# Optimization experiments

Measured on AMD Instinct MI355X. Metric: run time of the kernel, lower is better.

The kernel has to match this reference:

```python
import jax, jax.numpy as jnp
import numpy as np

H = 16  # n_heads (from init_kwargs)


def l2norm(x, eps=1e-6):
    return x * jax.lax.rsqrt(jnp.sum(x * x, axis=-1, keepdims=True) + eps)


def causal_conv1d(x, w, b):
    # depthwise causal conv: x (B,T,D), w (D,k), b (D,). Matches torch
    # Conv1d(d,d,k,groups=d,padding=k-1) followed by [:, :, :T] truncation.
    T = x.shape[1]
    k = w.shape[1]
    xp = jnp.pad(x, ((0, 0), (k - 1, 0), (0, 0)))
    y = b
    for j in range(k):  # k=4 taps, fixed small loop
        y = y + xp[:, j:j + T, :] * w[:, j]
    return y


def setup_inputs():
    key = jax.random.key(0)
    ks = jax.random.split(key, 16)
    B, T, D, kc = 2, 2048, 1024, 4
    d = D // H
    s = 1.0 / np.sqrt(D)
    return {
        "x": jax.random.normal(ks[0], (B, T, D), jnp.float32),
        "Wq": jax.random.normal(ks[1], (D, D), jnp.float32) * s,
        "Wk": jax.random.normal(ks[2], (D, D), jnp.float32) * s,
        "Wv": jax.random.normal(ks[3], (D, D), jnp.float32) * s,
        "Wo": jax.random.normal(ks[4], (D, D), jnp.float32) * s,
        "Wg": jax.random.normal(ks[5], (D, D), jnp.float32) * s,
        "Wb": jax.random.normal(ks[6], (D, H), jnp.float32) * s,
        "cq_w": jax.random.normal(ks[7], (D, kc), jnp.float32) * 0.3,
        "cq_b": jax.random.normal(ks[8], (D,), jnp.float32) * 0.1,
        "ck_w": jax.random.normal(ks[9], (D, kc), jnp.float32) * 0.3,
        "ck_b": jax.random.normal(ks[10], (D,), jnp.float32) * 0.1,
        "cv_w": jax.random.normal(ks[11], (D, kc), jnp.float32) * 0.3,
        "cv_b": jax.random.normal(ks[12], (D,), jnp.float32) * 0.1,
        "nw": jnp.ones((d,), jnp.float32),
    }


def reference(x, Wq, Wk, Wv, Wo, Wg, Wb, cq_w, cq_b, ck_w, ck_b, cv_w, cv_b, nw):
    B, T, D = x.shape
    d = D // H
    q = l2norm(jax.nn.silu(causal_conv1d(x @ Wq, cq_w, cq_b)).reshape(B, T, H, d))
    q = q / jnp.sqrt(jnp.asarray(d, x.dtype))
    k = l2norm(jax.nn.silu(causal_conv1d(x @ Wk, ck_w, ck_b)).reshape(B, T, H, d))
    v = jax.nn.silu(causal_conv1d(x @ Wv, cv_w, cv_b)).reshape(B, T, H, d)
    gate = (x @ Wg).reshape(B, T, H, d)
    beta = jax.nn.sigmoid(x @ Wb)[..., None]  # (B,T,H,1)

    def step(S, qkvb):
        q_t, k_t, v_t, b_t = qkvb  # (B,H,d), (B,H,d), (B,H,d), (B,H,1)
        err = (v_t - jnp.einsum('bhk,bhkv->bhv', k_t, S)) * b_t
        S = S + jnp.einsum('bhk,bhv->bhkv', k_t, err)
        o_t = jnp.einsum('bhk,bhkv->bhv', q_t, S)
        return S, o_t

    S0 = jnp.zeros((B, H, d, d), x.dtype)
    xs = (q.transpose(1, 0, 2, 3), k.transpose(1, 0, 2, 3),
          v.transpose(1, 0, 2, 3), beta.transpose(1, 0, 2, 3))
    _, oT = jax.lax.scan(step, S0, xs)
    o = oT.transpose(1, 0, 2, 3)  # (B,T,H,d)
    # RMSNorm over head_dim
    o = o * jax.lax.rsqrt(jnp.mean(o * o, axis=-1, keepdims=True) + 1e-5) * nw
    o = o * jax.nn.silu(gate)
    return o.reshape(B, T, D) @ Wo
```

## Files before the change

### kernel.cpp

```cpp
#include <hip/hip_runtime.h>
#include <hip/hip_bf16.h>

typedef __attribute__((ext_vector_type(8))) short short8;
typedef __attribute__((ext_vector_type(4))) float f32x4;

#define TSEQ 2048
#define DMODEL 1024
#define NH 16
#define HD 64
#define PLANE 4194304

__device__ __forceinline__ ushort f2bf(float f) {
    union { float f; unsigned int u; } c; c.f = f;
    unsigned int u = c.u + 0x7fffu + ((c.u >> 16) & 1u);
    return (ushort)(u >> 16);
}

__device__ __forceinline__ float bf2f(ushort u) {
    union { unsigned int i; float f; } c; c.i = ((unsigned int)u) << 16;
    return c.f;
}

__device__ __forceinline__ void split2(float x, ushort& h, ushort& l) {
    h = f2bf(x);
    float r = x - bf2f(h);
    l = f2bf(r);
}

__device__ __forceinline__ float silu_f(float y) {
    return y / (1.f + __expf(-y));
}

__device__ __forceinline__ void gl_lds16(const float* g, float* l) {
    __builtin_amdgcn_global_load_lds(
        (__attribute__((address_space(1))) void*)g,
        (__attribute__((address_space(3))) void*)l, 16, 0, 0);
}
__device__ __forceinline__ void gl_lds16u(const ushort* g, ushort* l) {
    __builtin_amdgcn_global_load_lds(
        (__attribute__((address_space(1))) void*)g,
        (__attribute__((address_space(3))) void*)l, 16, 0, 0);
}

__global__ void gdn_cvt_x(const float* __restrict__ x, ushort* __restrict__ xb) {
    int i = blockIdx.x * 256 + threadIdx.x;
    float4 v = ((const float4*)x)[i];
    ushort4 o;
    o.x = f2bf(v.x); o.y = f2bf(v.y); o.z = f2bf(v.z); o.w = f2bf(v.w);
    ((ushort4*)xb)[i] = o;
}

__global__ void gdn_cvt_w(const float* __restrict__ Wq, const float* __restrict__ Wk,
                          const float* __restrict__ Wv, const float* __restrict__ Wg,
                          const float* __restrict__ Wo, ushort* __restrict__ wt) {
    __shared__ float tile[32][33];
    int z = blockIdx.z;
    const float* W = (z == 0) ? Wq : (z == 1) ? Wk : (z == 2) ? Wv : (z == 3) ? Wg : Wo;
    int n0 = blockIdx.x * 32, k0 = blockIdx.y * 32;
    int tx = threadIdx.x, ty = threadIdx.y;
    #pragma unroll
    for (int j = 0; j < 32; j += 8)
        tile[ty + j][tx] = W[(size_t)(k0 + ty + j) * DMODEL + n0 + tx];
    __syncthreads();
    ushort* o = wt + (size_t)z * DMODEL * DMODEL;
    #pragma unroll
    for (int j = 0; j < 32; j += 8)
        o[(size_t)(n0 + ty + j) * DMODEL + k0 + tx] = f2bf(tile[tx][ty + j]);
}

__global__ void gdn_beta(const float* __restrict__ x, const float* __restrict__ Wb,
                         float* __restrict__ betaT) {
    __shared__ float xs[16][DMODEL];
    int tid = threadIdx.x;
    int m0 = blockIdx.x * 16;
    #pragma unroll
    for (int i = 0; i < 16; i++) {
        int idx = i * 256 + tid;
        int row = idx >> 8, c4 = idx & 255;
        *(float4*)&xs[row][c4 * 4] =
            *(const float4*)&x[(size_t)(m0 + row) * DMODEL + c4 * 4];
    }
    __syncthreads();
    int h = tid & 15, mi = tid >> 4;
    float acc = 0.f;
    for (int k = 0; k < DMODEL; ++k)
        acc += xs[mi][k] * Wb[k * NH + h];
    int m = m0 + mi;
    int b = m >> 11, t = m & (TSEQ - 1);
    betaT[((b * NH + h) << 11) + t] = 1.f / (1.f + __expf(-acc));
}

#define BK 32
__global__ __launch_bounds__(256) void gdn_gemm(const ushort* __restrict__ A,
                                                const ushort* __restrict__ Bt,
                                                float* __restrict__ outF,
                                                size_t planeStride) {
    __shared__ ushort As[128 * BK];
    __shared__ ushort Bs[128 * BK];
    int tid = threadIdx.x;
    int lane = tid & 63, wid = tid >> 6;
    int wm = wid & 1, wn = wid >> 1;
    int l15 = lane & 15, quad = lane >> 4;
    int bm = blockIdx.x, bn = blockIdx.y;
    const int K = DMODEL;

    int e0 = wid, e1 = wid + 4;
    int srow0 = e0 * 16 + (lane >> 2), srow1 = e1 * 16 + (lane >> 2);
    int scol = (lane & 3) * 8;
    const ushort* Ag0 = A + (size_t)(bm * 128 + srow0) * K + scol;
    const ushort* Ag1 = A + (size_t)(bm * 128 + srow1) * K + scol;
    const ushort* Bg0 = Bt + (size_t)(bn * 128 + srow0) * K + scol;
    const ushort* Bg1 = Bt + (size_t)(bn * 128 + srow1) * K + scol;
    ushort* Al0 = As + e0 * 512;
    ushort* Al1 = As + e1 * 512;
    ushort* Bl0 = Bs + e0 * 512;
    ushort* Bl1 = Bs + e1 * 512;

    f32x4 acc[4][4];
    #pragma unroll
    for (int i = 0; i < 4; i++)
        #pragma unroll
        for (int j = 0; j < 4; j++)
            acc[i][j] = (f32x4){0.f, 0.f, 0.f, 0.f};

    for (int kt = 0; kt < K; kt += BK) {
        __syncthreads();
        gl_lds16u(Ag0 + kt, Al0);
        gl_lds16u(Ag1 + kt, Al1);
        gl_lds16u(Bg0 + kt, Bl0);
        gl_lds16u(Bg1 + kt, Bl1);
        __syncthreads();
        short8 af[4], bf[4];
        #pragma unroll
        for (int i = 0; i < 4; i++) {
            af[i] = *(const short8*)&As[(wm * 64 + i * 16 + l15) * BK + quad * 8];
            bf[i] = *(const short8*)&Bs[(wn * 64 + i * 16 + l15) * BK + quad * 8];
        }
        #pragma unroll
        for (int mt = 0; mt < 4; mt++)
            #pragma unroll
            for (int nt = 0; nt < 4; nt++)
                acc[mt][nt] = __builtin_amdgcn_mfma_f32_16x16x32_bf16(
                    af[mt], bf[nt], acc[mt][nt], 0, 0, 0);
    }

    #pragma unroll
    for (int mt = 0; mt < 4; mt++)
        #pragma unroll
        for (int nt = 0; nt < 4; nt++)
            #pragma unroll
            for (int r = 0; r < 4; r++) {
                int row = bm * 128 + wm * 64 + mt * 16 + quad * 4 + r;
                int col = bn * 128 + wn * 64 + nt * 16 + l15;
                outF[(size_t)(col >> 10) * planeStride + (size_t)row * 1024 + (col & 1023)]
                    = acc[mt][nt][r];
            }
}

__global__ void gdn_conv(const float* __restrict__ pre,
                         const float* __restrict__ cqw, const float* __restrict__ cqb,
                         const float* __restrict__ ckw, const float* __restrict__ ckb,
                         const float* __restrict__ cvw, const float* __restrict__ cvb,
                         float* __restrict__ qn, float* __restrict__ kn, float* __restrict__ vn) {
    int m = blockIdx.x;
    int which = blockIdx.y;
    int t = m & (TSEQ - 1);
    const float* cw = (which == 0) ? cqw : (which == 1) ? ckw : cvw;
    const float* cb = (which == 0) ? cqb : (which == 1) ? ckb : cvb;
    float* dst = (which == 0) ? qn : (which == 1) ? kn : vn;
    int c = threadIdx.x * 4;

    float w[4][4];
    #pragma unroll
    for (int i = 0; i < 4; i++) {
        float4 t4 = ((const float4*)cw)[c + i];
        w[i][0] = t4.x; w[i][1] = t4.y; w[i][2] = t4.z; w[i][3] = t4.w;
    }
    float4 bias = ((const float4*)cb)[threadIdx.x];
    float y[4] = {bias.x, bias.y, bias.z, bias.w};

    const float* src = pre + (size_t)which * PLANE + (size_t)m * DMODEL + c;
    #pragma unroll
    for (int j = 0; j < 4; j++) {
        int tt = t - 3 + j;
        if (tt >= 0) {
            float4 xv = *(const float4*)(src + (long)(j - 3) * DMODEL);
            y[0] += xv.x * w[0][j];
            y[1] += xv.y * w[1][j];
            y[2] += xv.z * w[2][j];
            y[3] += xv.w * w[3][j];
        }
    }
    #pragma unroll
    for (int i = 0; i < 4; i++) y[i] = silu_f(y[i]);

    if (which < 2) {
        float ss = y[0]*y[0] + y[1]*y[1] + y[2]*y[2] + y[3]*y[3];
        ss += __shfl_xor(ss, 1);
        ss += __shfl_xor(ss, 2);
        ss += __shfl_xor(ss, 4);
        ss += __shfl_xor(ss, 8);
        float sc = rsqrtf(ss + 1e-6f);
        if (which == 0) sc *= 0.125f;
        #pragma unroll
        for (int i = 0; i < 4; i++) y[i] *= sc;
    }
    float4 o; o.x = y[0]; o.y = y[1]; o.z = y[2]; o.w = y[3];
    ((float4*)(dst + (size_t)m * 1024))[threadIdx.x] = o;
}

__global__ __launch_bounds__(256) void gdn_chunk(
    const float* __restrict__ kn, const float* __restrict__ vn,
    const float* __restrict__ betaT,
    ushort* __restrict__ WTst, ushort* __restrict__ U0st,
    float* __restrict__ Pst, float* __restrict__ Rst)
{
    __shared__ ushort Khi[64 * 72], Klo[64 * 72];
    __shared__ ushort KThi[64 * 72], KTlo[64 * 72];
    __shared__ ushort XThi[128 * 72], XTlo[128 * 72];
    __shared__ ushort Mneghi[64 * 72], Mneglo[64 * 72];
    __shared__ float  Xf[64 * 132];
    __shared__ float  MmDiag[4 * 16 * 20];
    __shared__ float  bet[64];

    int c = blockIdx.x, bh = blockIdx.y;
    int b = bh >> 4, h = bh & 15;
    int tid = threadIdx.x;
    int w = tid >> 6, lane = tid & 63;
    int l15 = lane & 15, quad = lane >> 4;
    size_t gbase = ((size_t)(b * TSEQ + c * 64)) * DMODEL + h * 64;
    size_t u = (size_t)bh * 32 + c;

    if (tid < 64) bet[tid] = betaT[((size_t)bh << 11) + c * 64 + tid];
    #pragma unroll
    for (int i = 0; i < 18; i++) {
        ((uint*)XThi)[tid + 256 * i] = 0u;
        ((uint*)XTlo)[tid + 256 * i] = 0u;
    }
    __syncthreads();

    #pragma unroll
    for (int i = 0; i < 4; i++) {
        int idx = tid + 256 * i;
        int r = idx >> 4, c4 = (idx & 15) * 4;
        float4 kv = *(const float4*)&kn[gbase + (size_t)r * DMODEL + c4];
        float4 vv = *(const float4*)&vn[gbase + (size_t)r * DMODEL + c4];
        float br = bet[r];
        float4 xk; xk.x = br * kv.x; xk.y = br * kv.y; xk.z = br * kv.z; xk.w = br * kv.w;
        float4 xv; xv.x = br * vv.x; xv.y = br * vv.y; xv.z = br * vv.z; xv.w = br * vv.w;
        *(float4*)&Xf[r * 132 + c4] = xk;
        *(float4*)&Xf[r * 132 + 64 + c4] = xv;
        ushort h0, l0, h1, l1, h2, l2, h3, l3;
        split2(kv.x, h0, l0); split2(kv.y, h1, l1);
        split2(kv.z, h2, l2); split2(kv.w, h3, l3);
        ((uint*)&Khi[r * 72 + c4])[0] = (uint)h0 | ((uint)h1 << 16);
        ((uint*)&Khi[r * 72 + c4])[1] = (uint)h2 | ((uint)h3 << 16);
        ((uint*)&Klo[r * 72 + c4])[0] = (uint)l0 | ((uint)l1 << 16);
        ((uint*)&Klo[r * 72 + c4])[1] = (uint)l2 | ((uint)l3 << 16);
        KThi[(c4 + 0) * 72 + r] = h0; KThi[(c4 + 1) * 72 + r] = h1;
        KThi[(c4 + 2) * 72 + r] = h2; KThi[(c4 + 3) * 72 + r] = h3;
        KTlo[(c4 + 0) * 72 + r] = l0; KTlo[(c4 + 1) * 72 + r] = l1;
        KTlo[(c4 + 2) * 72 + r] = l2; KTlo[(c4 + 3) * 72 + r] = l3;
    }
    __syncthreads();

    {
        f32x4 mAcc[4];
        #pragma unroll
        for (int tn = 0; tn < 4; tn++) mAcc[tn] = (f32x4){0.f, 0.f, 0.f, 0.f};
        #pragma unroll
        for (int ks = 0; ks < 2; ks++) {
            short8 aH = *(const short8*)&Khi[(16 * w + l15) * 72 + ks * 32 + quad * 8];
            short8 aL = *(const short8*)&Klo[(16 * w + l15) * 72 + ks * 32 + quad * 8];
            #pragma unroll
            for (int tn = 0; tn < 4; tn++) {
                short8 bH = *(const short8*)&Khi[(16 * tn + l15) * 72 + ks * 32 + quad * 8];
                short8 bL = *(const short8*)&Klo[(16 * tn + l15) * 72 + ks * 32 + quad * 8];
                mAcc[tn] = __builtin_amdgcn_mfma_f32_16x16x32_bf16(aH, bH, mAcc[tn], 0, 0, 0);
                mAcc[tn] = __builtin_amdgcn_mfma_f32_16x16x32_bf16(aH, bL, mAcc[tn], 0, 0, 0);
                mAcc[tn] = __builtin_amdgcn_mfma_f32_16x16x32_bf16(aL, bH, mAcc[tn], 0, 0, 0);
            }
        }
        #pragma unroll
        for (int tn = 0; tn < 4; tn++) {
            #pragma unroll
            for (int r = 0; r < 4; r++) {
                int row = 16 * w + quad * 4 + r;
                int col = tn * 16 + l15;
                float val = mAcc[tn][r] * bet[row];
                ushort hh = 0, ll = 0;
                if (col < row) {
                    float nv = -val;
                    hh = f2bf(nv);
                    ll = f2bf(nv - bf2f(hh));
                }
                Mneghi[row * 72 + col] = hh;
                Mneglo[row * 72 + col] = ll;
                if (tn == w) MmDiag[w * 320 + (row & 15) * 20 + l15] = val;
            }
        }
    }
    __syncthreads();

    #pragma unroll 1
    for (int st = 0; st < 4; st++) {
        int tb = st * 16;
        if (st) {
            f32x4 acc2[2];
            #pragma unroll
            for (int e = 0; e < 2; e++) {
                int tn = 2 * w + e;
                #pragma unroll
                for (int r = 0; r < 4; r++)
                    acc2[e][r] = Xf[(tb + quad * 4 + r) * 132 + tn * 16 + l15];
            }
            #pragma unroll
            for (int ks = 0; ks < 2; ks++) {
                short8 aH = *(const short8*)&Mneghi[(tb + l15) * 72 + ks * 32 + quad * 8];
                short8 aL = *(const short8*)&Mneglo[(tb + l15) * 72 + ks * 32 + quad * 8];
                #pragma unroll
                for (int e = 0; e < 2; e++) {
                    int tn = 2 * w + e;
                    short8 bH = *(const short8*)&XThi[(tn * 16 + l15) * 72 + ks * 32 + quad * 8];
                    short8 bL = *(const short8*)&XTlo[(tn * 16 + l15) * 72 + ks * 32 + quad * 8];
                    acc2[e] = __builtin_amdgcn_mfma_f32_16x16x32_bf16(aH, bH, acc2[e], 0, 0, 0);
                    acc2[e] = __builtin_amdgcn_mfma_f32_16x16x32_bf16(aH, bL, acc2[e], 0, 0, 0);
                    acc2[e] = __builtin_amdgcn_mfma_f32_16x16x32_bf16(aL, bH, acc2[e], 0, 0, 0);
                }
            }
            #pragma unroll
            for (int e = 0; e < 2; e++) {
                int tn = 2 * w + e;
                #pragma unroll
                for (int r = 0; r < 4; r++)
                    Xf[(tb + quad * 4 + r) * 132 + tn * 16 + l15] = acc2[e][r];
            }
        }
        __syncthreads();

        if (tid < 128) {
            const int j = tid;
            const float* MD = &MmDiag[st * 320];
            float xr[16];
            #pragma unroll
            for (int sb = 0; sb < 4; sb++) {
                float b4[4];
                #pragma unroll
                for (int i = 0; i < 4; i++)
                    b4[i] = Xf[(tb + sb * 4 + i) * 132 + j];
                #pragma unroll
                for (int u4 = 0; u4 < sb; u4++) {
                    #pragma unroll
                    for (int i = 0; i < 4; i++) {
                        float4 m4 = *(const float4*)&MD[(sb * 4 + i) * 20 + u4 * 4];
                        b4[i] -= m4.x * xr[u4 * 4 + 0] + m4.y * xr[u4 * 4 + 1]
                               + m4.z * xr[u4 * 4 + 2] + m4.w * xr[u4 * 4 + 3];
                    }
                }
                float x0 = b4[0];
                float x1 = b4[1] - MD[(sb * 4 + 1) * 20 + sb * 4 + 0] * x0;
                float x2 = b4[2] - MD[(sb * 4 + 2) * 20 + sb * 4 + 0] * x0
                                 - MD[(sb * 4 + 2) * 20 + sb * 4 + 1] * x1;
                float x3 = b4[3] - MD[(sb * 4 + 3) * 20 + sb * 4 + 0] * x0
                                 - MD[(sb * 4 + 3) * 20 + sb * 4 + 1] * x1
                                 - MD[(sb * 4 + 3) * 20 + sb * 4 + 2] * x2;
                xr[sb * 4 + 0] = x0; xr[sb * 4 + 1] = x1;
                xr[sb * 4 + 2] = x2; xr[sb * 4 + 3] = x3;
            }
            ushort hs[16], ls[16];
            #pragma unroll
            for (int i = 0; i < 16; i++) split2(xr[i], hs[i], ls[i]);
            uint4 ph0, ph1, pl0, pl1;
            ph0.x = (uint)hs[0] | ((uint)hs[1] << 16);  ph0.y = (uint)hs[2] | ((uint)hs[3] << 16);
            ph0.z = (uint)hs[4] | ((uint)hs[5] << 16);  ph0.w = (uint)hs[6] | ((uint)hs[7] << 16);
            ph1.x = (uint)hs[8] | ((uint)hs[9] << 16);  ph1.y = (uint)hs[10] | ((uint)hs[11] << 16);
            ph1.z = (uint)hs[12] | ((uint)hs[13] << 16); ph1.w = (uint)hs[14] | ((uint)hs[15] << 16);
            pl0.x = (uint)ls[0] | ((uint)ls[1] << 16);  pl0.y = (uint)ls[2] | ((uint)ls[3] << 16);
            pl0.z = (uint)ls[4] | ((uint)ls[5] << 16);  pl0.w = (uint)ls[6] | ((uint)ls[7] << 16);
            pl1.x = (uint)ls[8] | ((uint)ls[9] << 16);  pl1.y = (uint)ls[10] | ((uint)ls[11] << 16);
            pl1.z = (uint)ls[12] | ((uint)ls[13] << 16); pl1.w = (uint)ls[14] | ((uint)ls[15] << 16);
            *(uint4*)&XThi[j * 72 + tb] = ph0;  *(uint4*)&XThi[j * 72 + tb + 8] = ph1;
            *(uint4*)&XTlo[j * 72 + tb] = pl0;  *(uint4*)&XTlo[j * 72 + tb + 8] = pl1;
            if (j < 64) {
                ushort* wdst = WTst + u * 4096 + j * 64 + tb;
                *(uint4*)wdst = ph0; *(uint4*)(wdst + 8) = ph1;
            } else {
                ushort* udst = U0st + u * 4096 + (size_t)tb * 64 + (j - 64);
                #pragma unroll
                for (int i = 0; i < 16; i++) udst[i * 64] = hs[i];
            }
        }
        __syncthreads();
    }

    {
        f32x4 pAcc[4], rAcc[4];
        #pragma unroll
        for (int tn = 0; tn < 4; tn++) {
            pAcc[tn] = (f32x4){0.f, 0.f, 0.f, 0.f};
            rAcc[tn] = (f32x4){0.f, 0.f, 0.f, 0.f};
        }
        #pragma unroll
        for (int ks = 0; ks < 2; ks++) {
            short8 aH = *(const short8*)&XThi[(16 * w + l15) * 72 + ks * 32 + quad * 8];
            short8 aL = *(const short8*)&XTlo[(16 * w + l15) * 72 + ks * 32 + quad * 8];
            short8 cH = *(const short8*)&KThi[(16 * w + l15) * 72 + ks * 32 + quad * 8];
            short8 cL = *(const short8*)&KTlo[(16 * w + l15) * 72 + ks * 32 + quad * 8];
            #pragma unroll
            for (int tn = 0; tn < 4; tn++) {
                short8 bH = *(const short8*)&KThi[(16 * tn + l15) * 72 + ks * 32 + quad * 8];
                short8 bL = *(const short8*)&KTlo[(16 * tn + l15) * 72 + ks * 32 + quad * 8];
                pAcc[tn] = __builtin_amdgcn_mfma_f32_16x16x32_bf16(aH, bH, pAcc[tn], 0, 0, 0);
                pAcc[tn] = __builtin_amdgcn_mfma_f32_16x16x32_bf16(aH, bL, pAcc[tn], 0, 0, 0);
                pAcc[tn] = __builtin_amdgcn_mfma_f32_16x16x32_bf16(aL, bH, pAcc[tn], 0, 0, 0);
                short8 uH = *(const short8*)&XThi[(64 + 16 * tn + l15) * 72 + ks * 32 + quad * 8];
                short8 uL = *(const short8*)&XTlo[(64 + 16 * tn + l15) * 72 + ks * 32 + quad * 8];
                rAcc[tn] = __builtin_amdgcn_mfma_f32_16x16x32_bf16(cH, uH, rAcc[tn], 0, 0, 0);
                rAcc[tn] = __builtin_amdgcn_mfma_f32_16x16x32_bf16(cH, uL, rAcc[tn], 0, 0, 0);
                rAcc[tn] = __builtin_amdgcn_mfma_f32_16x16x32_bf16(cL, uH, rAcc[tn], 0, 0, 0);
            }
        }
        float* Po = Pst + u * 4096;
        float* Ro = Rst + u * 4096;
        #pragma unroll
        for (int tn = 0; tn < 4; tn++) {
            #pragma unroll
            for (int r = 0; r < 4; r++) {
                int row = 16 * w + quad * 4 + r;
                int col = tn * 16 + l15;
                Po[row * 64 + col] = pAcc[tn][r];
                Ro[col * 64 + row] = rAcc[tn][r];
            }
        }
    }
}

__global__ __launch_bounds__(256) void gdn_sstep(const float* __restrict__ Pst,
                                                 const float* __restrict__ Rst,
                                                 float* __restrict__ S0st)
{
    __shared__ float PTl[3][4096];
    __shared__ float Rl[3][1024];
    __shared__ float SshT[2][16][72];

    int bh = blockIdx.x >> 2, cg = blockIdx.x & 3;
    int tid = threadIdx.x;
    int t0 = (tid & 15) * 4;
    int j  = tid >> 4;
    int jg = cg * 16 + j;
    int wv = tid >> 6, ln = tid & 63;

    size_t ubase = (size_t)bh * 32 * 4096;

    *(float4*)&SshT[0][j][t0] = (float4){0.f, 0.f, 0.f, 0.f};

    #pragma unroll
    for (int t = 0; t < 2; t++) {
        size_t ub = ubase + (size_t)t * 4096;
        #pragma unroll
        for (int q = 0; q < 4; q++)
            gl_lds16(Pst + ub + (wv * 4 + q) * 256 + ln * 4, &PTl[t][(wv * 4 + q) * 256]);
        gl_lds16(Rst + ub + cg * 1024 + wv * 256 + ln * 4, &Rl[t][wv * 256]);
    }
    asm volatile("s_waitcnt vmcnt(5)" ::: "memory");
    asm volatile("s_waitcnt lgkmcnt(0)" ::: "memory");
    __builtin_amdgcn_s_barrier();

    int cur3 = 0;
    #pragma unroll 1
    for (int c = 0; c < 32; ++c) {
        int cur = c & 1, nxt = cur ^ 1;
        if (c + 2 < 32) {
            int b3 = cur3 + 2; if (b3 >= 3) b3 -= 3;
            size_t ub2 = ubase + (size_t)(c + 2) * 4096;
            #pragma unroll
            for (int q = 0; q < 4; q++)
                gl_lds16(Pst + ub2 + (wv * 4 + q) * 256 + ln * 4, &PTl[b3][(wv * 4 + q) * 256]);
            gl_lds16(Rst + ub2 + cg * 1024 + wv * 256 + ln * 4, &Rl[b3][wv * 256]);
        }
        float4 sold = *(const float4*)&SshT[cur][j][t0];
        size_t ub = ubase + (size_t)c * 4096;
        S0st[ub + (size_t)(t0 + 0) * 64 + jg] = sold.x;
        S0st[ub + (size_t)(t0 + 1) * 64 + jg] = sold.y;
        S0st[ub + (size_t)(t0 + 2) * 64 + jg] = sold.z;
        S0st[ub + (size_t)(t0 + 3) * 64 + jg] = sold.w;
        float4 racc = *(const float4*)&Rl[cur3][j * 64 + t0];
        float sub0 = 0.f, sub1 = 0.f, sub2 = 0.f, sub3 = 0.f;
        #pragma unroll
        for (int u4 = 0; u4 < 16; u4++) {
            float4 sv = *(const float4*)&SshT[cur][j][u4 * 4];
            #pragma unroll
            for (int e = 0; e < 4; e++) {
                float4 pt = *(const float4*)&PTl[cur3][(u4 * 4 + e) * 64 + t0];
                float s1 = (e == 0) ? sv.x : (e == 1) ? sv.y : (e == 2) ? sv.z : sv.w;
                sub0 = fmaf(pt.x, s1, sub0);
                sub1 = fmaf(pt.y, s1, sub1);
                sub2 = fmaf(pt.z, s1, sub2);
                sub3 = fmaf(pt.w, s1, sub3);
            }
        }
        float4 snew;
        snew.x = sold.x + racc.x - sub0;
        snew.y = sold.y + racc.y - sub1;
        snew.z = sold.z + racc.z - sub2;
        snew.w = sold.w + racc.w - sub3;
        *(float4*)&SshT[nxt][j][t0] = snew;
        if (c == 0)       { asm volatile("s_waitcnt vmcnt(9)"  ::: "memory"); }
        else if (c < 30)  { asm volatile("s_waitcnt vmcnt(13)" ::: "memory"); }
        else if (c == 30) { asm volatile("s_waitcnt vmcnt(8)"  ::: "memory"); }
        asm volatile("s_waitcnt lgkmcnt(0)" ::: "memory");
        __builtin_amdgcn_s_barrier();
        cur3 += 1; if (cur3 >= 3) cur3 -= 3;
    }
}

__global__ __launch_bounds__(256) void gdn_opass(
    const float* __restrict__ qn, const float* __restrict__ kn,
    const float* __restrict__ S0st, const ushort* __restrict__ WTst,
    const ushort* __restrict__ U0st, float* __restrict__ otmp2)
{
    __shared__ float Qs[64][65];
    __shared__ float KE[64][65];
    __shared__ float S0s[64][65];
    __shared__ float GT[4096];
    __shared__ ushort Wu[4096];
    __shared__ ushort Uu[4096];

    int c = blockIdx.x, bh = blockIdx.y;
    int b = bh >> 4, h = bh & 15;
    int tid = threadIdx.x;
    size_t gbase = ((size_t)(b * TSEQ + c * 64)) * DMODEL + h * 64;
    size_t u = (size_t)bh * 32 + c;

    #pragma unroll
    for (int i = 0; i < 4; i++) {
        int idx = tid + 256 * i;
        int r = idx >> 4, d4 = (idx & 15) * 4;
        float4 qv = *(const float4*)&qn[gbase + (size_t)r * DMODEL + d4];
        float4 kv = *(const float4*)&kn[gbase + (size_t)r * DMODEL + d4];
        float4 sv = *(const float4*)&S0st[u * 4096 + (size_t)idx * 4];
        Qs[r][d4 + 0] = qv.x; Qs[r][d4 + 1] = qv.y; Qs[r][d4 + 2] = qv.z; Qs[r][d4 + 3] = qv.w;
        KE[r][d4 + 0] = kv.x; KE[r][d4 + 1] = kv.y; KE[r][d4 + 2] = kv.z; KE[r][d4 + 3] = kv.w;
        S0s[r][d4 + 0] = sv.x; S0s[r][d4 + 1] = sv.y; S0s[r][d4 + 2] = sv.z; S0s[r][d4 + 3] = sv.w;
    }
    #pragma unroll
    for (int i = 0; i < 2; i++) {
        int idx = tid + 256 * i;
        uint4 w8 = *(const uint4*)&WTst[u * 4096 + (size_t)idx * 8];
        uint4 u8 = *(const uint4*)&U0st[u * 4096 + (size_t)idx * 8];
        *(uint4*)&Wu[idx * 8] = w8;
        *(uint4*)&Uu[idx * 8] = u8;
    }
    __syncthreads();

    int t0 = (tid & 15) * 4, s0 = (tid >> 4) * 4;

    float g[4][4];
    #pragma unroll
    for (int i = 0; i < 4; i++)
        #pragma unroll
        for (int j = 0; j < 4; j++) g[i][j] = 0.f;
    #pragma unroll 8
    for (int kk = 0; kk < 64; kk++) {
        float qt[4], kt[4];
        #pragma unroll
        for (int i = 0; i < 4; i++) qt[i] = Qs[t0 + i][kk];
        #pragma unroll
        for (int j = 0; j < 4; j++) kt[j] = KE[s0 + j][kk];
        #pragma unroll
        for (int i = 0; i < 4; i++)
            #pragma unroll
            for (int j = 0; j < 4; j++) g[i][j] = fmaf(qt[i], kt[j], g[i][j]);
    }
    float e[4][4];
    #pragma unroll
    for (int i = 0; i < 4; i++)
        #pragma unroll
        for (int j = 0; j < 4; j++) e[i][j] = 0.f;
    #pragma unroll 8
    for (int uu = 0; uu < 64; uu++) {
        ushort4 wv = *(const ushort4*)&Wu[uu * 64 + t0];
        float w0 = bf2f(wv.x), w1 = bf2f(wv.y), w2 = bf2f(wv.z), w3 = bf2f(wv.w);
        float s4[4];
        #pragma unroll
        for (int j = 0; j < 4; j++) s4[j] = S0s[uu][s0 + j];
        #pragma unroll
        for (int j = 0; j < 4; j++) {
            e[0][j] = fmaf(w0, s4[j], e[0][j]);
            e[1][j] = fmaf(w1, s4[j], e[1][j]);
            e[2][j] = fmaf(w2, s4[j], e[2][j]);
            e[3][j] = fmaf(w3, s4[j], e[3][j]);
        }
    }
    #pragma unroll
    for (int i = 0; i < 4; i++)
        #pragma unroll
        for (int jj = 0; jj < 4; jj++)
            GT[(s0 + jj) * 64 + t0 + i] = (s0 + jj <= t0 + i) ? g[i][jj] : 0.f;
    __syncthreads();
    #pragma unroll
    for (int i = 0; i < 4; i++) {
        ushort4 uv = *(const ushort4*)&Uu[(t0 + i) * 64 + s0];
        KE[t0 + i][s0 + 0] = bf2f(uv.x) - e[i][0];
        KE[t0 + i][s0 + 1] = bf2f(uv.y) - e[i][1];
        KE[t0 + i][s0 + 2] = bf2f(uv.z) - e[i][2];
        KE[t0 + i][s0 + 3] = bf2f(uv.w) - e[i][3];
    }
    __syncthreads();

    float o[4][4];
    #pragma unroll
    for (int i = 0; i < 4; i++)
        #pragma unroll
        for (int j = 0; j < 4; j++) o[i][j] = 0.f;
    #pragma unroll 8
    for (int kk = 0; kk < 64; kk++) {
        float qt[4], s4[4];
        #pragma unroll
        for (int i = 0; i < 4; i++) qt[i] = Qs[t0 + i][kk];
        #pragma unroll
        for (int j = 0; j < 4; j++) s4[j] = S0s[kk][s0 + j];
        #pragma unroll
        for (int i = 0; i < 4; i++)
            #pragma unroll
            for (int j = 0; j < 4; j++) o[i][j] = fmaf(qt[i], s4[j], o[i][j]);
    }
    #pragma unroll 8
    for (int ss = 0; ss < 64; ss++) {
        float4 gt = *(const float4*)&GT[ss * 64 + t0];
        float e4[4];
        #pragma unroll
        for (int j = 0; j < 4; j++) e4[j] = KE[ss][s0 + j];
        #pragma unroll
        for (int j = 0; j < 4; j++) {
            o[0][j] = fmaf(gt.x, e4[j], o[0][j]);
            o[1][j] = fmaf(gt.y, e4[j], o[1][j]);
            o[2][j] = fmaf(gt.z, e4[j], o[2][j]);
            o[3][j] = fmaf(gt.w, e4[j], o[3][j]);
        }
    }
    size_t obase = ((size_t)bh * 16 + (s0 >> 2)) * TSEQ + c * 64;
    #pragma unroll
    for (int i = 0; i < 4; i++) {
        float4 ov; ov.x = o[i][0]; ov.y = o[i][1]; ov.z = o[i][2]; ov.w = o[i][3];
        ((float4*)otmp2)[obase + t0 + i] = ov;
    }
}

__global__ void gdn_fuse(const float* __restrict__ otmp2, const float* __restrict__ pre,
                         const float* __restrict__ nw, ushort* __restrict__ ofused) {
    int m = blockIdx.x;
    int b = m >> 11, t = m & (TSEQ - 1);
    int tid = threadIdx.x;
    float4 o = ((const float4*)otmp2)[((size_t)((b * NH + (tid >> 4)) * 16 + (tid & 15))) * TSEQ + t];
    float ss = o.x*o.x + o.y*o.y + o.z*o.z + o.w*o.w;
    ss += __shfl_xor(ss, 1);
    ss += __shfl_xor(ss, 2);
    ss += __shfl_xor(ss, 4);
    ss += __shfl_xor(ss, 8);
    float r = rsqrtf(ss * (1.f / 64.f) + 1e-5f);
    float4 nwv = ((const float4*)nw)[tid & 15];
    float4 g = ((const float4*)(pre + 3 * (size_t)PLANE + (size_t)m * DMODEL))[tid];
    ushort4 out;
    out.x = f2bf(o.x * r * nwv.x * silu_f(g.x));
    out.y = f2bf(o.y * r * nwv.y * silu_f(g.y));
    out.z = f2bf(o.z * r * nwv.z * silu_f(g.z));
    out.w = f2bf(o.w * r * nwv.w * silu_f(g.w));
    ((ushort4*)ofused)[m * 256 + tid] = out;
}

extern "C" void kernel_launch(void* const* d_in, const int* in_sizes, int n_in,
                              void* d_out, int out_size, void* d_ws, size_t ws_size,
                              hipStream_t stream) {
    const float* x    = (const float*)d_in[0];
    const float* Wq   = (const float*)d_in[1];
    const float* Wk   = (const float*)d_in[2];
    const float* Wv   = (const float*)d_in[3];
    const float* Wo   = (const float*)d_in[4];
    const float* Wg   = (const float*)d_in[5];
    const float* Wb   = (const float*)d_in[6];
    const float* cq_w = (const float*)d_in[7];
    const float* cq_b = (const float*)d_in[8];
    const float* ck_w = (const float*)d_in[9];
    const float* ck_b = (const float*)d_in[10];
    const float* cv_w = (const float*)d_in[11];
    const float* cv_b = (const float*)d_in[12];
    const float* nw   = (const float*)d_in[13];

    char* ws = (char*)d_ws;
    ushort* xb     = (ushort*)(ws);
    ushort* wt     = (ushort*)(ws + 8388608);
    float*  pre    = (float*)(ws + 18874368);
    float*  qn     = (float*)(ws + 85983232);
    float*  kn     = (float*)(ws + 102760448);
    float*  vn     = (float*)(ws + 119537664);
    float*  betaT  = (float*)(ws + 136314880);
    float*  otmp2  = (float*)(ws + 136577024);
    ushort* ofused = (ushort*)(ws + 153354240);

    float*  Pst  = pre;
    float*  Rst  = pre + PLANE;
    float*  S0st = pre + 2 * PLANE;
    ushort* WTst = xb;
    ushort* U0st = ofused;

    gdn_cvt_x<<<4096, 256, 0, stream>>>(x, xb);
    gdn_cvt_w<<<dim3(32, 32, 5), dim3(32, 8), 0, stream>>>(Wq, Wk, Wv, Wg, Wo, wt);
    gdn_beta<<<256, 256, 0, stream>>>(x, Wb, betaT);
    gdn_gemm<<<dim3(32, 32), 256, 0, stream>>>(xb, wt, pre, (size_t)PLANE);
    gdn_conv<<<dim3(4096, 3), 256, 0, stream>>>(pre, cq_w, cq_b, ck_w, ck_b, cv_w, cv_b,
                                                qn, kn, vn);
    gdn_chunk<<<dim3(32, 32), 256, 0, stream>>>(kn, vn, betaT, WTst, U0st, Pst, Rst);
    gdn_sstep<<<128, 256, 0, stream>>>(Pst, Rst, S0st);
    gdn_opass<<<dim3(32, 32), 256, 0, stream>>>(qn, kn, S0st, WTst, U0st, otmp2);
    gdn_fuse<<<4096, 256, 0, stream>>>(otmp2, pre, nw, ofused);
    gdn_gemm<<<dim3(32, 8), 256, 0, stream>>>(ofused, wt + 4 * 1024 * 1024,
                                              (float*)d_out, (size_t)0);
}
```

Baseline: 428.4 us.

## Port chunk output pass to bf16 MFMA with split hi/lo precision

Replaces the scalar FP32 FMA matmuls in the gdn_opass kernel (QK^T, W·S0, Q·S0 and G·E) with 16x16x32 bf16 MFMA instructions. Each FP32 operand is split into hi and lo bf16 parts, and three cross products are accumulated to keep near-FP32 accuracy. Shared memory is repacked into padded bf16 tiles, with transposed layouts and reuse of buffers for G and E. The W input is negated with a sign-bit XOR so that U − W·S accumulates directly. This adds conversion work and scattered transposed LDS stores, and the otmp2 output store becomes less coalesced.

```diff
diff --git a/kernel.cpp b/kernel.cpp
--- a/kernel.cpp
+++ b/kernel.cpp
@@ -519,131 +519,140 @@
     const float* __restrict__ S0st, const ushort* __restrict__ WTst,
     const ushort* __restrict__ U0st, float* __restrict__ otmp2)
 {
-    __shared__ float Qs[64][65];
-    __shared__ float KE[64][65];
-    __shared__ float S0s[64][65];
-    __shared__ float GT[4096];
-    __shared__ ushort Wu[4096];
-    __shared__ ushort Uu[4096];
+    __shared__ ushort pool[36864];
+    ushort* Qhi  = pool;
+    ushort* Qlo  = pool + 4608;
+    ushort* Khi  = pool + 2 * 4608;
+    ushort* Klo  = pool + 3 * 4608;
+    ushort* SThi = pool + 4 * 4608;
+    ushort* STlo = pool + 5 * 4608;
+    ushort* Wn   = pool + 6 * 4608;
+    ushort* Uu   = pool + 7 * 4608;
+    ushort* Ghi  = Qhi;  ushort* Glo  = Qlo;
+    ushort* EThi = Khi;  ushort* ETlo = Klo;
 
     int c = blockIdx.x, bh = blockIdx.y;
     int b = bh >> 4, h = bh & 15;
     int tid = threadIdx.x;
+    int w = tid >> 6, lane = tid & 63;
+    int l15 = lane & 15, quad = lane >> 4;
     size_t gbase = ((size_t)(b * TSEQ + c * 64)) * DMODEL + h * 64;
     size_t u = (size_t)bh * 32 + c;
 
     #pragma unroll
     for (int i = 0; i < 4; i++) {
         int idx = tid + 256 * i;
-        int r = idx >> 4, d4 = (idx & 15) * 4;
-        float4 qv = *(const float4*)&qn[gbase + (size_t)r * DMODEL + d4];
-        float4 kv = *(const float4*)&kn[gbase + (size_t)r * DMODEL + d4];
+        int r = idx >> 4, c4 = (idx & 15) * 4;
+        float4 qv = *(const float4*)&qn[gbase + (size_t)r * DMODEL + c4];
+        float4 kv = *(const float4*)&kn[gbase + (size_t)r * DMODEL + c4];
         float4 sv = *(const float4*)&S0st[u * 4096 + (size_t)idx * 4];
-        Qs[r][d4 + 0] = qv.x; Qs[r][d4 + 1] = qv.y; Qs[r][d4 + 2] = qv.z; Qs[r][d4 + 3] = qv.w;
-        KE[r][d4 + 0] = kv.x; KE[r][d4 + 1] = kv.y; KE[r][d4 + 2] = kv.z; KE[r][d4 + 3] = kv.w;
-        S0s[r][d4 + 0] = sv.x; S0s[r][d4 + 1] = sv.y; S0s[r][d4 + 2] = sv.z; S0s[r][d4 + 3] = sv.w;
+        ushort h0, l0, h1, l1, h2, l2, h3, l3;
+        split2(qv.x, h0, l0); split2(qv.y, h1, l1);
+        split2(qv.z, h2, l2); split2(qv.w, h3, l3);
+        ((uint*)&Qhi[r * 72 + c4])[0] = (uint)h0 | ((uint)h1 << 16);
+        ((uint*)&Qhi[r * 72 + c4])[1] = (uint)h2 | ((uint)h3 << 16);
+        ((uint*)&Qlo[r * 72 + c4])[0] = (uint)l0 | ((uint)l1 << 16);
+        ((uint*)&Qlo[r * 72 + c4])[1] = (uint)l2 | ((uint)l3 << 16);
+        split2(kv.x, h0, l0); split2(kv.y, h1, l1);
+        split2(kv.z, h2, l2); split2(kv.w, h3, l3);
+        ((uint*)&Khi[r * 72 + c4])[0] = (uint)h0 | ((uint)h1 << 16);
+        ((uint*)&Khi[r * 72 + c4])[1] = (uint)h2 | ((uint)h3 << 16);
+        ((uint*)&Klo[r * 72 + c4])[0] = (uint)l0 | ((uint)l1 << 16);
+        ((uint*)&Klo[r * 72 + c4])[1] = (uint)l2 | ((uint)l3 << 16);
+        split2(sv.x, h0, l0); split2(sv.y, h1, l1);
+        split2(sv.z, h2, l2); split2(sv.w, h3, l3);
+        SThi[(c4 + 0) * 72 + r] = h0; STlo[(c4 + 0) * 72 + r] = l0;
+        SThi[(c4 + 1) * 72 + r] = h1; STlo[(c4 + 1) * 72 + r] = l1;
+        SThi[(c4 + 2) * 72 + r] = h2; STlo[(c4 + 2) * 72 + r] = l2;
+        SThi[(c4 + 3) * 72 + r] = h3; STlo[(c4 + 3) * 72 + r] = l3;
     }
     #pragma unroll
     for (int i = 0; i < 2; i++) {
         int idx = tid + 256 * i;
-        uint4 w8 = *(const uint4*)&WTst[u * 4096 + (size_t)idx * 8];
-        uint4 u8 = *(const uint4*)&U0st[u * 4096 + (size_t)idx * 8];
-        *(uint4*)&Wu[idx * 8] = w8;
-        *(uint4*)&Uu[idx * 8] = u8;
+        uint4 w8 = ((const uint4*)(WTst + u * 4096))[idx];
+        int ur = idx >> 3, t8 = (idx & 7) * 8;
+        uint v0 = w8.x ^ 0x80008000u, v1 = w8.y ^ 0x80008000u;
+        uint v2 = w8.z ^ 0x80008000u, v3 = w8.w ^ 0x80008000u;
+        Wn[(t8 + 0) * 72 + ur] = (ushort)v0; Wn[(t8 + 1) * 72 + ur] = (ushort)(v0 >> 16);
+        Wn[(t8 + 2) * 72 + ur] = (ushort)v1; Wn[(t8 + 3) * 72 + ur] = (ushort)(v1 >> 16);
+        Wn[(t8 + 4) * 72 + ur] = (ushort)v2; Wn[(t8 + 5) * 72 + ur] = (ushort)(v2 >> 16);
+        Wn[(t8 + 6) * 72 + ur] = (ushort)v3; Wn[(t8 + 7) * 72 + ur] = (ushort)(v3 >> 16);
+        ((uint4*)Uu)[idx] = ((const uint4*)(U0st + u * 4096))[idx];
     }
     __syncthreads();
 
-    int t0 = (tid & 15) * 4, s0 = (tid >> 4) * 4;
-
-    float g[4][4];
-    #pragma unroll
-    for (int i = 0; i < 4; i++)
-        #pragma unroll
-        for (int j = 0; j < 4; j++) g[i][j] = 0.f;
-    #pragma unroll 8
-    for (int kk = 0; kk < 64; kk++) {
-        float qt[4], kt[4];
-        #pragma unroll
-        for (int i = 0; i < 4; i++) qt[i] = Qs[t0 + i][kk];
-        #pragma unroll
-        for (int j = 0; j < 4; j++) kt[j] = KE[s0 + j][kk];
-        #pragma unroll
-        for (int i = 0; i < 4; i++)
-            #pragma unroll
-            for (int j = 0; j < 4; j++) g[i][j] = fmaf(qt[i], kt[j], g[i][j]);
-    }
-    float e[4][4];
-    #pragma unroll
-    for (int i = 0; i < 4; i++)
-        #pragma unroll
-        for (int j = 0; j < 4; j++) e[i][j] = 0.f;
-    #pragma unroll 8
-    for (int uu = 0; uu < 64; uu++) {
-        ushort4 wv = *(const ushort4*)&Wu[uu * 64 + t0];
-        float w0 = bf2f(wv.x), w1 = bf2f(wv.y), w2 = bf2f(wv.z), w3 = bf2f(wv.w);
-        float s4[4];
-        #pragma unroll
-        for (int j = 0; j < 4; j++) s4[j] = S0s[uu][s0 + j];
-        #pragma unroll
-        for (int j = 0; j < 4; j++) {
-            e[0][j] = fmaf(w0, s4[j], e[0][j]);
-            e[1][j] = fmaf(w1, s4[j], e[1][j]);
-            e[2][j] = fmaf(w2, s4[j], e[2][j]);
-            e[3][j] = fmaf(w3, s4[j], e[3][j]);
-        }
-    }
-    #pragma unroll
-    for (int i = 0; i < 4; i++)
-        #pragma unroll
-        for (int jj = 0; jj < 4; jj++)
-            GT[(s0 + jj) * 64 + t0 + i] = (s0 + jj <= t0 + i) ? g[i][jj] : 0.f;
+    f32x4 accG[4], accO[4], accE[4];
+    #pragma unroll
+    for (int tn = 0; tn < 4; tn++) {
+        accG[tn] = (f32x4){0.f, 0.f, 0.f, 0.f};
+        accO[tn] = (f32x4){0.f, 0.f, 0.f, 0.f};
+        #pragma unroll
+        for (int r = 0; r < 4; r++)
+            accE[tn][r] = bf2f(Uu[(16 * w + quad * 4 + r) * 64 + tn * 16 + l15]);
+    }
+    #pragma unroll
+    for (int ks = 0; ks < 2; ks++) {
+        int ko = ks * 32 + quad * 8;
+        short8 qH = *(const short8*)&Qhi[(16 * w + l15) * 72 + ko];
+        short8 qL = *(const short8*)&Qlo[(16 * w + l15) * 72 + ko];
+        short8 wA = *(const short8*)&Wn [(16 * w + l15) * 72 + ko];
+        #pragma unroll
+        for (int tn = 0; tn < 4; tn++) {
+            short8 kH = *(const short8*)&Khi [(16 * tn + l15) * 72 + ko];
+            short8 kL = *(const short8*)&Klo [(16 * tn + l15) * 72 + ko];
+            short8 sH = *(const short8*)&SThi[(16 * tn + l15) * 72 + ko];
+            short8 sL = *(const short8*)&STlo[(16 * tn + l15) * 72 + ko];
+            accG[tn] = __builtin_amdgcn_mfma_f32_16x16x32_bf16(qH, kH, accG[tn], 0, 0, 0);
+            accG[tn] = __builtin_amdgcn_mfma_f32_16x16x32_bf16(qH, kL, accG[tn], 0, 0, 0);
+            accG[tn] = __builtin_amdgcn_mfma_f32_16x16x32_bf16(qL, kH, accG[tn], 0, 0, 0);
+            accO[tn] = __builtin_amdgcn_mfma_f32_16x16x32_bf16(qH, sH, accO[tn], 0, 0, 0);
+            accO[tn] = __builtin_amdgcn_mfma_f32_16x16x32_bf16(qH, sL, accO[tn], 0, 0, 0);
+            accO[tn] = __builtin_amdgcn_mfma_f32_16x16x32_bf16(qL, sH, accO[tn], 0, 0, 0);
+            accE[tn] = __builtin_amdgcn_mfma_f32_16x16x32_bf16(wA, sH, accE[tn], 0, 0, 0);
+            accE[tn] = __builtin_amdgcn_mfma_f32_16x16x32_bf16(wA, sL, accE[tn], 0, 0, 0);
+        }
+    }
     __syncthreads();
-    #pragma unroll
-    for (int i = 0; i < 4; i++) {
-        ushort4 uv = *(const ushort4*)&Uu[(t0 + i) * 64 + s0];
-        KE[t0 + i][s0 + 0] = bf2f(uv.x) - e[i][0];
-        KE[t0 + i][s0 + 1] = bf2f(uv.y) - e[i][1];
-        KE[t0 + i][s0 + 2] = bf2f(uv.z) - e[i][2];
-        KE[t0 + i][s0 + 3] = bf2f(uv.w) - e[i][3];
+
+    #pragma unroll
+    for (int tn = 0; tn < 4; tn++) {
+        #pragma unroll
+        for (int r = 0; r < 4; r++) {
+            int row = 16 * w + quad * 4 + r;
+            int col = tn * 16 + l15;
+            float gv = (col <= row) ? accG[tn][r] : 0.f;
+            ushort gh, gl; split2(gv, gh, gl);
+            Ghi[row * 72 + col] = gh; Glo[row * 72 + col] = gl;
+            ushort eh, el; split2(accE[tn][r], eh, el);
+            EThi[col * 72 + row] = eh; ETlo[col * 72 + row] = el;
+        }
     }
     __syncthreads();
 
-    float o[4][4];
-    #pragma unroll
-    for (int i = 0; i < 4; i++)
-        #pragma unroll
-        for (int j = 0; j < 4; j++) o[i][j] = 0.f;
-    #pragma unroll 8
-    for (int kk = 0; kk < 64; kk++) {
-        float qt[4], s4[4];
-        #pragma unroll
-        for (int i = 0; i < 4; i++) qt[i] = Qs[t0 + i][kk];
-        #pragma unroll
-        for (int j = 0; j < 4; j++) s4[j] = S0s[kk][s0 + j];
-        #pragma unroll
-        for (int i = 0; i < 4; i++)
-            #pragma unroll
-            for (int j = 0; j < 4; j++) o[i][j] = fmaf(qt[i], s4[j], o[i][j]);
-    }
-    #pragma unroll 8
-    for (int ss = 0; ss < 64; ss++) {
-        float4 gt = *(const float4*)&GT[ss * 64 + t0];
-        float e4[4];
-        #pragma unroll
-        for (int j = 0; j < 4; j++) e4[j] = KE[ss][s0 + j];
-        #pragma unroll
-        for (int j = 0; j < 4; j++) {
-            o[0][j] = fmaf(gt.x, e4[j], o[0][j]);
-            o[1][j] = fmaf(gt.y, e4[j], o[1][j]);
-            o[2][j] = fmaf(gt.z, e4[j], o[2][j]);
-            o[3][j] = fmaf(gt.w, e4[j], o[3][j]);
-        }
-    }
-    size_t obase = ((size_t)bh * 16 + (s0 >> 2)) * TSEQ + c * 64;
-    #pragma unroll
-    for (int i = 0; i < 4; i++) {
-        float4 ov; ov.x = o[i][0]; ov.y = o[i][1]; ov.z = o[i][2]; ov.w = o[i][3];
-        ((float4*)otmp2)[obase + t0 + i] = ov;
+    #pragma unroll
+    for (int ks = 0; ks < 2; ks++) {
+        int ko = ks * 32 + quad * 8;
+        short8 gH = *(const short8*)&Ghi[(16 * w + l15) * 72 + ko];
+        short8 gL = *(const short8*)&Glo[(16 * w + l15) * 72 + ko];
+        #pragma unroll
+        for (int tn = 0; tn < 4; tn++) {
+            short8 eH = *(const short8*)&EThi[(16 * tn + l15) * 72 + ko];
+            short8 eL = *(const short8*)&ETlo[(16 * tn + l15) * 72 + ko];
+            accO[tn] = __builtin_amdgcn_mfma_f32_16x16x32_bf16(gH, eH, accO[tn], 0, 0, 0);
+            accO[tn] = __builtin_amdgcn_mfma_f32_16x16x32_bf16(gH, eL, accO[tn], 0, 0, 0);
+            accO[tn] = __builtin_amdgcn_mfma_f32_16x16x32_bf16(gL, eH, accO[tn], 0, 0, 0);
+        }
+    }
+
+    #pragma unroll
+    for (int tn = 0; tn < 4; tn++) {
+        #pragma unroll
+        for (int r = 0; r < 4; r++) {
+            int row = 16 * w + quad * 4 + r;
+            int col = tn * 16 + l15;
+            otmp2[(((size_t)bh * 16 + (col >> 2)) * TSEQ + c * 64 + row) * 4 + (col & 3)]
+                = accO[tn][r];
+        }
     }
 }
 
```

Measured after the change: 392.9 us. 8.3% less time.
